# Optimization experiments

Measured on AMD Instinct MI355X. Metric: run time of the kernel, lower is better.

## Reference

```python
import jax, jax.numpy as jnp
import numpy as np

D = 512
H = 16
DH = D // H
N = 1024
R0 = 10.0
K_ITER = 20
LAM = 1.0


def _ln(x, w=None, b=None, eps=1e-5):
    m = x.mean(-1, keepdims=True)
    v = ((x - m) ** 2).mean(-1, keepdims=True)
    y = (x - m) * jax.lax.rsqrt(v + eps)
    if w is not None:
        y = y * w + b
    return y


def setup_inputs() -> dict:
    key = jax.random.key(0)
    ks = jax.random.split(key, 24)
    s = 1.0 / np.sqrt(D)
    inp = {
        'h': jax.random.normal(ks[0], (N, D), jnp.float32),
        'x_res': jax.random.normal(ks[1], (N, 3), jnp.float32) * 5.0,
        'mu': jax.random.uniform(ks[2], (H, N), jnp.float32, 0.1, 1.0),
        'nu': jax.random.uniform(ks[3], (H, N), jnp.float32, 0.1, 1.0),
        'log_u_prev': jnp.zeros((H, N), jnp.float32),
        'log_v_prev': jnp.zeros((H, N), jnp.float32),
        'w_rel_res': jax.random.normal(ks[4], (H, N, N), jnp.float32) * 0.1,
        'w_dist': jax.random.uniform(ks[5], (H,), jnp.float32),
        'pos_bins': jax.random.randint(ks[6], (N, N), 0, 68),
        'geo_gate': jax.random.uniform(ks[7], (H,), jnp.float32),
        'ln_attn_w': jnp.ones((D,), jnp.float32),
        'ln_attn_b': jnp.zeros((D,), jnp.float32),
        'Wq': jax.random.normal(ks[8], (D, D), jnp.float32) * s,
        'Wk': jax.random.normal(ks[9], (D, D), jnp.float32) * s,
        'Wv': jax.random.normal(ks[10], (D, D), jnp.float32) * s,
        'Wg': jax.random.normal(ks[11], (D, D), jnp.float32) * s,
        'Wo': jax.random.normal(ks[12], (D, D), jnp.float32) * s,
        'gamma': jax.random.normal(ks[13], (H,), jnp.float32) * 0.01,
        'ln_ff_w': jnp.ones((D,), jnp.float32),
        'ln_ff_b': jnp.zeros((D,), jnp.float32),
        'W1': jax.random.normal(ks[14], (D, 4 * D), jnp.float32) * s,
        'W3': jax.random.normal(ks[15], (D, 4 * D), jnp.float32) * s,
        'W2': jax.random.normal(ks[16], (4 * D, D), jnp.float32) / np.sqrt(4 * D),
    }
    return inp


def reference(h, x_res, mu, nu, log_u_prev, log_v_prev, w_rel_res, w_dist,
              pos_bins, geo_gate, ln_attn_w, ln_attn_b, Wq, Wk, Wv, Wg, Wo,
              gamma, ln_ff_w, ln_ff_b, W1, W3, W2):
    n = h.shape[0]
    h_n = _ln(h, ln_attn_w, ln_attn_b)
    # projections -> (H, N, d_h)
    Q = (h_n @ Wq).reshape(n, H, DH).transpose(1, 0, 2)
    K = (h_n @ Wk).reshape(n, H, DH).transpose(1, 0, 2)
    V = (h_n @ Wv).reshape(n, H, DH).transpose(1, 0, 2)
    G = (h_n @ Wg).reshape(n, H, DH).transpose(1, 0, 2)
    Q_ln = _ln(Q)
    K_ln = _ln(K)
    content = -jnp.einsum('hid,hjd->hij', Q_ln, K_ln) / np.sqrt(DH)
    pos_bias = w_rel_res  # precomputed (H, N, N)
    d2 = ((x_res[:, None, :] - x_res[None, :, :]) ** 2).sum(-1)
    dist = jnp.sqrt(jnp.maximum(d2, 1e-12))
    f_dist = dist / (R0 + dist)
    eff_w = geo_gate * w_dist
    C = content + pos_bias + eff_w[:, None, None] * f_dist[None]
    # log-domain unbalanced Sinkhorn, per-head eps
    eps_h = jnp.array([0.5] * 4 + [1.0] * 4 + [2.0] * 4 + [4.0] * 4, jnp.float32)
    eps_b = eps_h[:, None, None]
    fac = (LAM / (LAM + eps_h))[:, None]  # (H, 1)
    log_mu = jnp.log(jnp.clip(mu, 1e-8))
    log_nu = jnp.log(jnp.clip(nu, 1e-8))
    M = -C / eps_b  # (H, N, N)

    def step(carry, _):
        lu, lv = carry
        lu = fac * (log_mu - jax.nn.logsumexp(M + lv[:, None, :], axis=2))
        lv = fac * (log_nu - jax.nn.logsumexp(M + lu[:, :, None], axis=1))
        return (lu, lv), None

    (log_u, log_v), _ = jax.lax.scan(jax.checkpoint(step),
                                     (log_u_prev, log_v_prev), None,
                                     length=K_ITER)
    # transport plan and outputs
    T = jnp.exp(M + log_u[:, :, None] + log_v[:, None, :])
    T_norm = T / (T.sum(-1, keepdims=True) + 1e-8)
    o = jax.nn.sigmoid(G) * jnp.einsum('hij,hjd->hid', T_norm, V)
    o = o.transpose(1, 0, 2).reshape(n, D)
    h = h + o @ Wo
    x_centroid = jnp.einsum('hij,jc->hic', T_norm, x_res)  # (H, N, 3)
    delta = x_res[None] - x_centroid
    x_res = x_res + jnp.einsum('h,hnc->nc', gamma, delta)
    # SwiGLU FFN
    ff = _ln(h, ln_ff_w, ln_ff_b)
    h = h + (jax.nn.silu(ff @ W1) * (ff @ W3)) @ W2
    return h, x_res, log_u, log_v
```

## Files before the change

### kernel.cpp

```cpp
#include <hip/hip_runtime.h>
#include <math.h>

#define NTOK 1024
#define DDIM 512

using short8 = __attribute__((ext_vector_type(8))) short;
using f32x4  = __attribute__((ext_vector_type(4))) float;

__device__ __forceinline__ float4 ld4(const float* p){ return *(const float4*)p; }
__device__ __forceinline__ void st4(float* p, float4 v){ *(float4*)p = v; }
__device__ __forceinline__ unsigned short bf16r(float x) {
  unsigned int u = __float_as_uint(x);
  u += 0x7fffu + ((u >> 16) & 1u);
  return (unsigned short)(u >> 16);
}
__device__ __forceinline__ float bf16f(unsigned short h) {
  return __uint_as_float(((unsigned int)h) << 16);
}
__device__ __forceinline__ f32x4 mfma16(short8 a, short8 b, f32x4 c) {
  return __builtin_amdgcn_mfma_f32_16x16x32_bf16(a, b, c, 0, 0, 0);
}

__global__ __launch_bounds__(256) void ln_rows(const float* __restrict__ x,
    const float* __restrict__ w, const float* __restrict__ b, float* __restrict__ y) {
  int row = blockIdx.x, t = threadIdx.x;
  const float* xr = x + ((size_t)row << 9);
  float v0 = xr[t], v1 = xr[t + 256];
  float s = v0 + v1, q = v0*v0 + v1*v1;
  #pragma unroll
  for (int off = 1; off < 64; off <<= 1) { s += __shfl_xor(s, off); q += __shfl_xor(q, off); }
  __shared__ float ls[4], lq[4], mb[2];
  int wv = t >> 6;
  if ((t & 63) == 0) { ls[wv] = s; lq[wv] = q; }
  __syncthreads();
  if (t == 0) {
    float S = ls[0]+ls[1]+ls[2]+ls[3];
    float Q = lq[0]+lq[1]+lq[2]+lq[3];
    float m = S * (1.f/512.f);
    float var = Q * (1.f/512.f) - m*m;
    mb[0] = m; mb[1] = 1.f / sqrtf(var + 1e-5f);
  }
  __syncthreads();
  float m = mb[0], inv = mb[1];
  float* yr = y + ((size_t)row << 9);
  yr[t]       = (v0 - m) * inv * w[t] + b[t];
  yr[t + 256] = (v1 - m) * inv * w[t + 256] + b[t + 256];
}

struct C4 {
  const float *S0, *S1, *S2, *S3;
  unsigned short *D0, *D1, *D2, *D3;
};
__global__ __launch_bounds__(256) void convT(C4 p, int K, int N) {
  __shared__ unsigned short Th[64][68];
  __shared__ unsigned short Tl[64][68];
  int z = blockIdx.z;
  const float* src = (z==0)?p.S0:(z==1)?p.S1:(z==2)?p.S2:p.S3;
  unsigned short* dst = (z==0)?p.D0:(z==1)?p.D1:(z==2)?p.D2:p.D3;
  int nt = blockIdx.x << 6, kt = blockIdx.y << 6;
  int t = threadIdx.x;
  int r = t >> 4, c4 = (t & 15) << 2;
  #pragma unroll
  for (int pp = 0; pp < 4; ++pp) {
    int kk = r + (pp << 4);
    float4 v = ld4(src + (size_t)(kt + kk) * N + nt + c4);
    float vv[4] = {v.x, v.y, v.z, v.w};
    #pragma unroll
    for (int i = 0; i < 4; ++i) {
      unsigned short h = bf16r(vv[i]);
      Th[c4 + i][kk] = h;
      Tl[c4 + i][kk] = bf16r(vv[i] - bf16f(h));
    }
  }
  __syncthreads();
  size_t loff = (size_t)N * K;
  #pragma unroll
  for (int pp = 0; pp < 4; ++pp) {
    int nn = r + (pp << 4);
    ushort4 oh, ol;
    oh.x = Th[nn][c4]; oh.y = Th[nn][c4+1]; oh.z = Th[nn][c4+2]; oh.w = Th[nn][c4+3];
    ol.x = Tl[nn][c4]; ol.y = Tl[nn][c4+1]; ol.z = Tl[nn][c4+2]; ol.w = Tl[nn][c4+3];
    *(ushort4*)(dst + (size_t)(nt + nn) * K + kt + c4) = oh;
    *(ushort4*)(dst + loff + (size_t)(nt + nn) * K + kt + c4) = ol;
  }
}

struct P4 {
  const unsigned short *W0, *W1, *W2, *W3;
  float *C0, *C1, *C2, *C3;
};
template<int MODE>
__global__ __launch_bounds__(256) void gemm_mfma(const float* __restrict__ A,
    P4 p, int Kd, int Nd, int kwin) {
  __shared__ unsigned short Ash[64][72];
  __shared__ unsigned short Asl[64][72];
  __shared__ unsigned short Bsh[64][72];
  __shared__ unsigned short Bsl[64][72];
  int t = threadIdx.x;
  int z = blockIdx.z;
  const unsigned short* W = (z==0)?p.W0:(z==1)?p.W1:(z==2)?p.W2:p.W3;
  float* C = (z==0)?p.C0:(z==1)?p.C1:(z==2)?p.C2:p.C3;
  const unsigned short* Wl = W + (size_t)Nd * Kd;
  int bm = blockIdx.y << 6, bn = blockIdx.x << 6;
  int wid = t >> 6, lane = t & 63;
  int wm = wid >> 1, wn = wid & 1;
  int lr = lane & 15, lk = lane >> 4;
  int r0 = t >> 3, ks = (t & 7) << 3;
  int kbeg = kwin ? z * kwin : 0;
  int kend = kwin ? kbeg + kwin : Kd;
  f32x4 acc[2][2];
  #pragma unroll
  for (int i = 0; i < 2; ++i)
    #pragma unroll
    for (int j = 0; j < 2; ++j)
      #pragma unroll
      for (int r = 0; r < 4; ++r) acc[i][j][r] = 0.f;
  for (int k0 = kbeg; k0 < kend; k0 += 64) {
    float4 a00 = ld4(A + (size_t)(bm + r0) * Kd + k0 + ks);
    float4 a01 = ld4(A + (size_t)(bm + r0) * Kd + k0 + ks + 4);
    float4 a10 = ld4(A + (size_t)(bm + r0 + 32) * Kd + k0 + ks);
    float4 a11 = ld4(A + (size_t)(bm + r0 + 32) * Kd + k0 + ks + 4);
    uint4 b0h = *(const uint4*)(W  + (size_t)(bn + r0) * Kd + k0 + ks);
    uint4 b1h = *(const uint4*)(W  + (size_t)(bn + r0 + 32) * Kd + k0 + ks);
    uint4 b0l = *(const uint4*)(Wl + (size_t)(bn + r0) * Kd + k0 + ks);
    uint4 b1l = *(const uint4*)(Wl + (size_t)(bn + r0 + 32) * Kd + k0 + ks);
    __syncthreads();
    {
      float va[8] = {a00.x,a00.y,a00.z,a00.w,a01.x,a01.y,a01.z,a01.w};
      short8 h8, l8;
      #pragma unroll
      for (int i = 0; i < 8; ++i) {
        unsigned short h = bf16r(va[i]);
        h8[i] = (short)h; l8[i] = (short)bf16r(va[i] - bf16f(h));
      }
      *(short8*)&Ash[r0][ks] = h8;
      *(short8*)&Asl[r0][ks] = l8;
    }
    {
      float va[8] = {a10.x,a10.y,a10.z,a10.w,a11.x,a11.y,a11.z,a11.w};
      short8 h8, l8;
      #pragma unroll
      for (int i = 0; i < 8; ++i) {
        unsigned short h = bf16r(va[i]);
        h8[i] = (short)h; l8[i] = (short)bf16r(va[i] - bf16f(h));
      }
      *(short8*)&Ash[r0 + 32][ks] = h8;
      *(short8*)&Asl[r0 + 32][ks] = l8;
    }
    *(uint4*)&Bsh[r0][ks] = b0h;
    *(uint4*)&Bsh[r0 + 32][ks] = b1h;
    *(uint4*)&Bsl[r0][ks] = b0l;
    *(uint4*)&Bsl[r0 + 32][ks] = b1l;
    __syncthreads();
    #pragma unroll
    for (int s = 0; s < 2; ++s) {
      short8 ah0 = *(const short8*)&Ash[wm*32 + lr][s*32 + lk*8];
      short8 ah1 = *(const short8*)&Ash[wm*32 + 16 + lr][s*32 + lk*8];
      short8 al0 = *(const short8*)&Asl[wm*32 + lr][s*32 + lk*8];
      short8 al1 = *(const short8*)&Asl[wm*32 + 16 + lr][s*32 + lk*8];
      short8 bh0 = *(const short8*)&Bsh[wn*32 + lr][s*32 + lk*8];
      short8 bh1 = *(const short8*)&Bsh[wn*32 + 16 + lr][s*32 + lk*8];
      short8 bl0 = *(const short8*)&Bsl[wn*32 + lr][s*32 + lk*8];
      short8 bl1 = *(const short8*)&Bsl[wn*32 + 16 + lr][s*32 + lk*8];
      acc[0][0] = mfma16(ah0, bh0, acc[0][0]);
      acc[0][1] = mfma16(ah0, bh1, acc[0][1]);
      acc[1][0] = mfma16(ah1, bh0, acc[1][0]);
      acc[1][1] = mfma16(ah1, bh1, acc[1][1]);
      acc[0][0] = mfma16(al0, bh0, acc[0][0]);
      acc[0][1] = mfma16(al0, bh1, acc[0][1]);
      acc[1][0] = mfma16(al1, bh0, acc[1][0]);
      acc[1][1] = mfma16(al1, bh1, acc[1][1]);
      acc[0][0] = mfma16(ah0, bl0, acc[0][0]);
      acc[0][1] = mfma16(ah0, bl1, acc[0][1]);
      acc[1][0] = mfma16(ah1, bl0, acc[1][0]);
      acc[1][1] = mfma16(ah1, bl1, acc[1][1]);
    }
  }
  #pragma unroll
  for (int fm = 0; fm < 2; ++fm)
    #pragma unroll
    for (int fn = 0; fn < 2; ++fn) {
      int n = bn + wn*32 + fn*16 + lr;
      #pragma unroll
      for (int r = 0; r < 4; ++r) {
        int m = bm + wm*32 + fm*16 + lk*4 + r;
        float v = acc[fm][fn][r];
        if (MODE == 0) {
          if (z < 3) C[(((size_t)(n >> 5) << 10) + m) * 32 + (n & 31)] = v;
          else       C[(size_t)m * Nd + n] = v;
        } else {
          C[(size_t)m * Nd + n] = v;
        }
      }
    }
}

__global__ __launch_bounds__(256) void qk_ln(float* __restrict__ Q, float* __restrict__ K) {
  float* P = blockIdx.y ? K : Q;
  int t = threadIdx.x;
  int row = blockIdx.x * 8 + (t >> 5);
  int l = t & 31;
  float* p = P + ((size_t)row << 5);
  float x = p[l];
  float s = x, q = x*x;
  #pragma unroll
  for (int off = 16; off; off >>= 1) { s += __shfl_xor(s, off, 32); q += __shfl_xor(q, off, 32); }
  float m = s * (1.f/32.f);
  float var = q * (1.f/32.f) - m*m;
  float inv = 1.f / sqrtf(var + 1e-5f);
  p[l] = (x - m) * inv;
}

__global__ __launch_bounds__(256) void build_M(const float* __restrict__ Qln,
    const float* __restrict__ Kln, const float* __restrict__ wrel,
    const float* __restrict__ xres, const float* __restrict__ wdist,
    const float* __restrict__ ggate, short* __restrict__ Mq) {
  int jt = blockIdx.x, it = blockIdx.y, h = blockIdx.z;
  int t = threadIdx.x;
  __shared__ float Qs[64][44], Ks[64][44];
  __shared__ float xi[64][4], xj[64][4];
  #pragma unroll
  for (int rep = 0; rep < 2; ++rep) {
    int idx = t + (rep << 8);
    int rr = idx >> 3, dq = (idx & 7) << 2;
    st4(&Qs[rr][dq], ld4(Qln + ((((size_t)h << 10) + (it << 6) + rr) << 5) + dq));
    st4(&Ks[rr][dq], ld4(Kln + ((((size_t)h << 10) + (jt << 6) + rr) << 5) + dq));
  }
  if (t < 64) {
    int gi = (it << 6) + t, gj = (jt << 6) + t;
    xi[t][0] = xres[gi*3]; xi[t][1] = xres[gi*3+1]; xi[t][2] = xres[gi*3+2];
    xj[t][0] = xres[gj*3]; xj[t][1] = xres[gj*3+1]; xj[t][2] = xres[gj*3+2];
  }
  __syncthreads();
  int g = h >> 2;
  float inv_eps = 2.0f / (float)(1 << g);
  float effw = ggate[h] * wdist[h];
  int tr = t >> 4, tc = t & 15;
  float acc[4][4] = {};
  #pragma unroll
  for (int d0 = 0; d0 < 32; d0 += 4) {
    float4 q4[4], k4[4];
    #pragma unroll
    for (int a = 0; a < 4; ++a) q4[a] = ld4(&Qs[(tr << 2) + a][d0]);
    #pragma unroll
    for (int bq = 0; bq < 4; ++bq) k4[bq] = ld4(&Ks[(tc << 2) + bq][d0]);
    #pragma unroll
    for (int a = 0; a < 4; ++a)
      #pragma unroll
      for (int bq = 0; bq < 4; ++bq)
        acc[a][bq] += q4[a].x*k4[bq].x + q4[a].y*k4[bq].y + q4[a].z*k4[bq].z + q4[a].w*k4[bq].w;
  }
  const float is32 = 0.17677669529663687f;
  #pragma unroll
  for (int a = 0; a < 4; ++a) {
    int il = (tr << 2) + a;
    int i = (it << 6) + il;
    float xa0 = xi[il][0], xa1 = xi[il][1], xa2 = xi[il][2];
    size_t base = ((size_t)h << 20) + ((size_t)i << 10) + (jt << 6) + (tc << 2);
    float4 w4 = ld4(wrel + base);
    short o16[4];
    #pragma unroll
    for (int bq = 0; bq < 4; ++bq) {
      int jl = (tc << 2) + bq;
      float dx = xa0 - xj[jl][0], dy = xa1 - xj[jl][1], dz = xa2 - xj[jl][2];
      float d2 = dx*dx + dy*dy + dz*dz;
      float dist = sqrtf(fmaxf(d2, 1e-12f));
      float f = dist / (10.0f + dist);
      float wv = (bq==0)?w4.x:(bq==1)?w4.y:(bq==2)?w4.z:w4.w;
      float m = (acc[a][bq] * is32 - wv - effw * f) * inv_eps;
      o16[bq] = (short)__float2int_rn(fminf(fmaxf(m * 256.f, -32000.f), 32000.f));
    }
    short4 q4o; q4o.x = o16[0]; q4o.y = o16[1]; q4o.z = o16[2]; q4o.w = o16[3];
    *(short4*)(Mq + base) = q4o;
  }
}

__global__ __launch_bounds__(256) void sink_iter16(const short* __restrict__ Mq,
    const float* __restrict__ lvb, const float* __restrict__ mu,
    float* __restrict__ lu_out, float* __restrict__ part) {
  __shared__ float lds[4][1024];
  __shared__ float logmu[32];
  int bt = blockIdx.x, h = blockIdx.y;
  int t = threadIdx.x, w = t >> 6, lane = t & 63;
  int g = h >> 2;
  float eps = 0.5f * (float)(1 << g);
  float fac = 1.f / (1.f + eps);
  const float qs = 1.f / 256.f;
  int rowbase = bt << 5;
  if (t < 32) logmu[t] = __logf(fmaxf(mu[(h << 10) + rowbase + t], 1e-8f));
  const short* Mh = Mq + ((size_t)h << 20);
  int ib = rowbase + (w << 3);
  short8 qa[8], qb[8];
  #pragma unroll
  for (int k = 0; k < 8; ++k) {
    const short* row = Mh + ((size_t)(ib + k) << 10) + (lane << 3);
    qa[k] = *(const short8*)row;
    qb[k] = *(const short8*)(row + 512);
  }
  float4 lv4[2][2], env[2][2];
  #pragma unroll
  for (int c = 0; c < 2; ++c) {
    const float* lp = lvb + (h << 10) + (c << 9) + (lane << 3);
    lv4[c][0] = ld4(lp);
    lv4[c][1] = ld4(lp + 4);
    #pragma unroll
    for (int hv = 0; hv < 2; ++hv) {
      env[c][hv].x = __expf(-lv4[c][hv].x); env[c][hv].y = __expf(-lv4[c][hv].y);
      env[c][hv].z = __expf(-lv4[c][hv].z); env[c][hv].w = __expf(-lv4[c][hv].w);
    }
  }
  float4 colacc[2][2];
  #pragma unroll
  for (int c = 0; c < 2; ++c)
    #pragma unroll
    for (int hv = 0; hv < 2; ++hv) colacc[c][hv] = make_float4(0.f,0.f,0.f,0.f);
  #pragma unroll
  for (int k = 0; k < 8; ++k) {
    short8 q0 = qa[k], q1 = qb[k];
    float4 e[2][2];
    e[0][0].x = __expf((float)q0[0]*qs + lv4[0][0].x);
    e[0][0].y = __expf((float)q0[1]*qs + lv4[0][0].y);
    e[0][0].z = __expf((float)q0[2]*qs + lv4[0][0].z);
    e[0][0].w = __expf((float)q0[3]*qs + lv4[0][0].w);
    e[0][1].x = __expf((float)q0[4]*qs + lv4[0][1].x);
    e[0][1].y = __expf((float)q0[5]*qs + lv4[0][1].y);
    e[0][1].z = __expf((float)q0[6]*qs + lv4[0][1].z);
    e[0][1].w = __expf((float)q0[7]*qs + lv4[0][1].w);
    e[1][0].x = __expf((float)q1[0]*qs + lv4[1][0].x);
    e[1][0].y = __expf((float)q1[1]*qs + lv4[1][0].y);
    e[1][0].z = __expf((float)q1[2]*qs + lv4[1][0].z);
    e[1][0].w = __expf((float)q1[3]*qs + lv4[1][0].w);
    e[1][1].x = __expf((float)q1[4]*qs + lv4[1][1].x);
    e[1][1].y = __expf((float)q1[5]*qs + lv4[1][1].y);
    e[1][1].z = __expf((float)q1[6]*qs + lv4[1][1].z);
    e[1][1].w = __expf((float)q1[7]*qs + lv4[1][1].w);
    float racc = ((e[0][0].x + e[0][0].y) + (e[0][0].z + e[0][0].w))
               + ((e[0][1].x + e[0][1].y) + (e[0][1].z + e[0][1].w))
               + ((e[1][0].x + e[1][0].y) + (e[1][0].z + e[1][0].w))
               + ((e[1][1].x + e[1][1].y) + (e[1][1].z + e[1][1].w));
    #pragma unroll
    for (int off = 1; off < 64; off <<= 1) racc += __shfl_xor(racc, off);
    float lu = fac * (logmu[(w << 3) + k] - __logf(racc));
    if (lane == 0) lu_out[(h << 10) + ib + k] = lu;
    float s1 = __expf(lu);
    #pragma unroll
    for (int c = 0; c < 2; ++c)
      #pragma unroll
      for (int hv = 0; hv < 2; ++hv) {
        colacc[c][hv].x += s1 * (e[c][hv].x * env[c][hv].x);
        colacc[c][hv].y += s1 * (e[c][hv].y * env[c][hv].y);
        colacc[c][hv].z += s1 * (e[c][hv].z * env[c][hv].z);
        colacc[c][hv].w += s1 * (e[c][hv].w * env[c][hv].w);
      }
  }
  #pragma unroll
  for (int c = 0; c < 2; ++c) {
    st4(&lds[w][(c << 9) + (lane << 3)], colacc[c][0]);
    st4(&lds[w][(c << 9) + (lane << 3) + 4], colacc[c][1]);
  }
  __syncthreads();
  #pragma unroll
  for (int c = 0; c < 4; ++c) {
    int j = t + (c << 8);
    float v = (lds[0][j] + lds[1][j]) + (lds[2][j] + lds[3][j]);
    part[(((size_t)(h << 5) + bt) << 10) + j] = v;
  }
}

__global__ __launch_bounds__(256) void sink_fin(const float* __restrict__ part,
    const float* __restrict__ nu, float* __restrict__ lvb) {
  int cx = blockIdx.x, h = blockIdx.y;
  int t = threadIdx.x;
  int g = h >> 2;
  float eps = 0.5f * (float)(1 << g);
  float fac = 1.f / (1.f + eps);
  int j = (cx << 8) + t;
  float sum = 0.f;
  #pragma unroll 8
  for (int b = 0; b < 32; ++b)
    sum += part[(((size_t)(h << 5) + b) << 10) + j];
  float lv = fac * (__logf(fmaxf(nu[(h << 10) + j], 1e-8f)) - __logf(sum));
  lvb[(h << 10) + j] = lv;
}

__global__ __launch_bounds__(256) void attn_out_v3(const short* __restrict__ Mq,
    const float* __restrict__ lu_g, const float* __restrict__ lv_g,
    const float* __restrict__ V, const float* __restrict__ G,
    const float* __restrict__ xres, float* __restrict__ o_buf, float* __restrict__ xc) {
  __shared__ short mslab[32][1024];
  __shared__ float lv_s[1024];
  __shared__ float Vs[64][40];
  int rb = blockIdx.x, h = blockIdx.y;
  int t = threadIdx.x;
  int rowbase = rb << 5;
  const short* Mh = Mq + ((size_t)h << 20) + ((size_t)rowbase << 10);
  #pragma unroll
  for (int rep = 0; rep < 16; ++rep) {
    int idx = (rep << 8) + t;
    int rr = idx >> 7, c8 = (idx & 127) << 3;
    *(short8*)&mslab[rr][c8] = *(const short8*)(Mh + ((size_t)rr << 10) + c8);
  }
  ((float4*)lv_s)[t] = ld4(lv_g + (h << 10) + (t << 2));
  int r = t >> 3, cg = t & 7;
  float lu_r = lu_g[(h << 10) + rowbase + r];
  const float qs = 1.f / 256.f;
  float accO[4] = {0.f, 0.f, 0.f, 0.f};
  float rs = 0.f, accX = 0.f;
  for (int jt = 0; jt < 16; ++jt) {
    __syncthreads();
    {
      int vr = t >> 2, dq = (t & 3) << 3;
      const float* vp = V + ((((size_t)h << 10) + (jt << 6) + vr) << 5) + dq;
      st4(&Vs[vr][dq], ld4(vp));
      st4(&Vs[vr][dq + 4], ld4(vp + 4));
    }
    if (t < 64) {
      int j = (jt << 6) + t;
      Vs[t][32] = xres[j*3]; Vs[t][33] = xres[j*3+1]; Vs[t][34] = xres[j*3+2];
    }
    __syncthreads();
    const short* mrow = &mslab[r][jt << 6];
    const float* lvp = &lv_s[jt << 6];
    #pragma unroll 8
    for (int jj = 0; jj < 64; ++jj) {
      float e = __expf((float)mrow[jj] * qs + lu_r + lvp[jj]);
      float4 v4 = ld4(&Vs[jj][cg << 2]);
      accO[0] += e*v4.x; accO[1] += e*v4.y; accO[2] += e*v4.z; accO[3] += e*v4.w;
      rs += e;
      accX += e * Vs[jj][32 + cg];
    }
  }
  float inv = 1.f / (rs + 1e-8f);
  int i = rowbase + r;
  size_t ga = ((size_t)i << 9) + (h << 5) + (cg << 2);
  float4 g4 = ld4(G + ga);
  float4 o;
  o.x = accO[0]*inv / (1.f + __expf(-g4.x));
  o.y = accO[1]*inv / (1.f + __expf(-g4.y));
  o.z = accO[2]*inv / (1.f + __expf(-g4.z));
  o.w = accO[3]*inv / (1.f + __expf(-g4.w));
  st4(o_buf + ga, o);
  if (cg < 3)
    xc[((size_t)((h << 10) + i)) * 3 + cg] = accX * inv;
}

__global__ void x_update(const float* __restrict__ xres, const float* __restrict__ xc,
    const float* __restrict__ gamma, float* __restrict__ xout) {
  int idx = blockIdx.x * 256 + threadIdx.x;
  if (idx >= 3072) return;
  float x = xres[idx];
  float s = x;
  #pragma unroll
  for (int hh = 0; hh < 16; ++hh) s += gamma[hh] * (x - xc[(size_t)hh * 3072 + idx]);
  xout[idx] = s;
}

__global__ __launch_bounds__(256) void silu_mul(const float* __restrict__ P1,
    const float* __restrict__ P3, float* __restrict__ AB) {
  int i = (blockIdx.x * 256 + threadIdx.x) << 2;
  float4 a = ld4(P1 + i), b = ld4(P3 + i);
  float4 o;
  o.x = a.x / (1.f + __expf(-a.x)) * b.x;
  o.y = a.y / (1.f + __expf(-a.y)) * b.y;
  o.z = a.z / (1.f + __expf(-a.z)) * b.z;
  o.w = a.w / (1.f + __expf(-a.w)) * b.w;
  st4(AB + i, o);
}

__global__ __launch_bounds__(256) void add3(const float* __restrict__ a,
    const float* __restrict__ b, const float* __restrict__ c, float* __restrict__ o) {
  int i = (blockIdx.x * 256 + threadIdx.x) << 2;
  float4 va = ld4(a + i), vb = ld4(b + i), vc = ld4(c + i);
  st4(o + i, make_float4(va.x+vb.x+vc.x, va.y+vb.y+vc.y, va.z+vb.z+vc.z, va.w+vb.w+vc.w));
}

extern "C" void kernel_launch(void* const* d_in, const int* in_sizes, int n_in,
                              void* d_out, int out_size, void* d_ws, size_t ws_size,
                              hipStream_t stream) {
  const float* h_in    = (const float*)d_in[0];
  const float* x_res   = (const float*)d_in[1];
  const float* mu      = (const float*)d_in[2];
  const float* nu      = (const float*)d_in[3];
  const float* lv_prev = (const float*)d_in[5];
  const float* wrel    = (const float*)d_in[6];
  const float* wdist   = (const float*)d_in[7];
  const float* ggate   = (const float*)d_in[9];
  const float* lnaw    = (const float*)d_in[10];
  const float* lnab    = (const float*)d_in[11];
  const float* Wq      = (const float*)d_in[12];
  const float* Wk      = (const float*)d_in[13];
  const float* Wv      = (const float*)d_in[14];
  const float* Wg      = (const float*)d_in[15];
  const float* Wo      = (const float*)d_in[16];
  const float* gamma   = (const float*)d_in[17];
  const float* lnfw    = (const float*)d_in[18];
  const float* lnfb    = (const float*)d_in[19];
  const float* W1      = (const float*)d_in[20];
  const float* W3      = (const float*)d_in[21];
  const float* W2      = (const float*)d_in[22];

  float* out = (float*)d_out;
  float* OUT_H  = out;
  float* OUT_X  = out + 524288;
  float* OUT_LU = out + 527360;
  float* OUT_LV = out + 543744;

  if (ws_size < (size_t)19988480 * sizeof(float)) return;
  float* ws   = (float*)d_ws;
  float* Qb   = ws;
  float* Kb   = ws + 524288;
  float* Vb   = ws + 1048576;
  float* Gb   = ws + 1572864;
  float* Mb   = ws + 2097152;
  float* part = ws + 18874368;
  float* xcb  = ws + 19922944;
  short* Mq   = (short*)Mb;
  float* h_n = Mb;
  unsigned short* WqT = (unsigned short*)(Mb + 524288);
  unsigned short* WkT = (unsigned short*)(Mb + 786432);
  unsigned short* WvT = (unsigned short*)(Mb + 1048576);
  unsigned short* WgT = (unsigned short*)(Mb + 1310720);
  float* P1 = Mb;
  float* P3 = Mb + 2097152;
  float* ABb = Mb + 4194304;
  unsigned short* W1T = (unsigned short*)(Mb + 6291456);
  unsigned short* W3T = (unsigned short*)(Mb + 7340032);
  unsigned short* W2T = (unsigned short*)(Mb + 8388608);
  unsigned short* WoT = (unsigned short*)(Mb + 9437184);
  float* Pa = Mb + 9699328;
  float* Pb = Mb + 10223616;
  float* o_buf = part;
  float* h2  = Qb;
  float* ffb = Kb;

  ln_rows<<<NTOK, 256, 0, stream>>>(h_in, lnaw, lnab, h_n);
  {
    C4 c = { Wq, Wk, Wv, Wg, WqT, WkT, WvT, WgT };
    convT<<<dim3(8, 8, 4), 256, 0, stream>>>(c, 512, 512);
  }
  {
    P4 p = { WqT, WkT, WvT, WgT, Qb, Kb, Vb, Gb };
    gemm_mfma<0><<<dim3(8, 16, 4), 256, 0, stream>>>(h_n, p, 512, 512, 0);
  }
  qk_ln<<<dim3(2048, 2), 256, 0, stream>>>(Qb, Kb);
  build_M<<<dim3(16, 16, 16), 256, 0, stream>>>(Qb, Kb, wrel, x_res, wdist, ggate, Mq);
  hipMemcpyAsync(OUT_LV, lv_prev, 16384 * sizeof(float), hipMemcpyDeviceToDevice, stream);
  for (int it = 0; it < 20; ++it) {
    sink_iter16<<<dim3(32, 16), 256, 0, stream>>>(Mq, OUT_LV, mu, OUT_LU, part);
    sink_fin<<<dim3(4, 16), 256, 0, stream>>>(part, nu, OUT_LV);
  }
  attn_out_v3<<<dim3(32, 16), 256, 0, stream>>>(Mq, OUT_LU, OUT_LV, Vb, Gb, x_res, o_buf, xcb);
  x_update<<<12, 256, 0, stream>>>(x_res, xcb, gamma, OUT_X);

  {
    C4 c = { Wo, nullptr, nullptr, nullptr, WoT, nullptr, nullptr, nullptr };
    convT<<<dim3(8, 8, 1), 256, 0, stream>>>(c, 512, 512);
  }
  {
    C4 c = { W1, W3, nullptr, nullptr, W1T, W3T, nullptr, nullptr };
    convT<<<dim3(32, 8, 2), 256, 0, stream>>>(c, 512, 2048);
  }
  {
    C4 c = { W2, nullptr, nullptr, nullptr, W2T, nullptr, nullptr, nullptr };
    convT<<<dim3(8, 32, 1), 256, 0, stream>>>(c, 2048, 512);
  }
  {
    P4 p = { WoT, WoT, nullptr, nullptr, Pa, Pb, nullptr, nullptr };
    gemm_mfma<1><<<dim3(8, 16, 2), 256, 0, stream>>>(o_buf, p, 512, 512, 256);
  }
  add3<<<512, 256, 0, stream>>>(Pa, Pb, h_in, h2);
  ln_rows<<<NTOK, 256, 0, stream>>>(h2, lnfw, lnfb, ffb);
  {
    P4 p = { W1T, W3T, nullptr, nullptr, P1, P3, nullptr, nullptr };
    gemm_mfma<1><<<dim3(32, 16, 2), 256, 0, stream>>>(ffb, p, 512, 2048, 0);
  }
  silu_mul<<<2048, 256, 0, stream>>>(P1, P3, ABb);
  {
    P4 p = { W2T, W2T, nullptr, nullptr, Pa, Pb, nullptr, nullptr };
    gemm_mfma<1><<<dim3(8, 16, 2), 256, 0, stream>>>(ABb, p, 2048, 512, 1024);
  }
  add3<<<512, 256, 0, stream>>>(Pa, Pb, h2, OUT_H);
}
```

Baseline: 492.3 us.

## Halve Sinkhorn rows per block and precompute bf16 exp slab in attention output

Measured after the change: 478.1 us. 2.9% less time.

```diff
diff --git a/kernel.cpp b/kernel.cpp
--- a/kernel.cpp
+++ b/kernel.cpp
@@ -275,24 +275,23 @@
   }
 }
 
-__global__ __launch_bounds__(256) void sink_iter16(const short* __restrict__ Mq,
+__global__ __launch_bounds__(256) void sink_iter8(const short* __restrict__ Mq,
     const float* __restrict__ lvb, const float* __restrict__ mu,
     float* __restrict__ lu_out, float* __restrict__ part) {
   __shared__ float lds[4][1024];
-  __shared__ float logmu[32];
+  __shared__ float logmu[16];
   int bt = blockIdx.x, h = blockIdx.y;
   int t = threadIdx.x, w = t >> 6, lane = t & 63;
-  int g = h >> 2;
-  float eps = 0.5f * (float)(1 << g);
+  float eps = 0.5f * (float)(1 << (h >> 2));
   float fac = 1.f / (1.f + eps);
   const float qs = 1.f / 256.f;
-  int rowbase = bt << 5;
-  if (t < 32) logmu[t] = __logf(fmaxf(mu[(h << 10) + rowbase + t], 1e-8f));
+  int rowbase = bt << 4;
+  if (t < 16) logmu[t] = __logf(fmaxf(mu[(h << 10) + rowbase + t], 1e-8f));
   const short* Mh = Mq + ((size_t)h << 20);
-  int ib = rowbase + (w << 3);
-  short8 qa[8], qb[8];
-  #pragma unroll
-  for (int k = 0; k < 8; ++k) {
+  int ib = rowbase + (w << 2);
+  short8 qa[4], qb[4];
+  #pragma unroll
+  for (int k = 0; k < 4; ++k) {
     const short* row = Mh + ((size_t)(ib + k) << 10) + (lane << 3);
     qa[k] = *(const short8*)row;
     qb[k] = *(const short8*)(row + 512);
@@ -315,7 +314,7 @@
     #pragma unroll
     for (int hv = 0; hv < 2; ++hv) colacc[c][hv] = make_float4(0.f,0.f,0.f,0.f);
   #pragma unroll
-  for (int k = 0; k < 8; ++k) {
+  for (int k = 0; k < 4; ++k) {
     short8 q0 = qa[k], q1 = qb[k];
     float4 e[2][2];
     e[0][0].x = __expf((float)q0[0]*qs + lv4[0][0].x);
@@ -340,7 +339,7 @@
                + ((e[1][1].x + e[1][1].y) + (e[1][1].z + e[1][1].w));
     #pragma unroll
     for (int off = 1; off < 64; off <<= 1) racc += __shfl_xor(racc, off);
-    float lu = fac * (logmu[(w << 3) + k] - __logf(racc));
+    float lu = fac * (logmu[(w << 2) + k] - __logf(racc));
     if (lane == 0) lu_out[(h << 10) + ib + k] = lu;
     float s1 = __expf(lu);
     #pragma unroll
@@ -363,7 +362,7 @@
   for (int c = 0; c < 4; ++c) {
     int j = t + (c << 8);
     float v = (lds[0][j] + lds[1][j]) + (lds[2][j] + lds[3][j]);
-    part[(((size_t)(h << 5) + bt) << 10) + j] = v;
+    part[(((size_t)(h << 6) + bt) << 10) + j] = v;
   }
 }
 
@@ -371,39 +370,46 @@
     const float* __restrict__ nu, float* __restrict__ lvb) {
   int cx = blockIdx.x, h = blockIdx.y;
   int t = threadIdx.x;
-  int g = h >> 2;
-  float eps = 0.5f * (float)(1 << g);
+  float eps = 0.5f * (float)(1 << (h >> 2));
   float fac = 1.f / (1.f + eps);
   int j = (cx << 8) + t;
   float sum = 0.f;
-  #pragma unroll 8
-  for (int b = 0; b < 32; ++b)
-    sum += part[(((size_t)(h << 5) + b) << 10) + j];
+  #pragma unroll 16
+  for (int b = 0; b < 64; ++b)
+    sum += part[(((size_t)(h << 6) + b) << 10) + j];
   float lv = fac * (__logf(fmaxf(nu[(h << 10) + j], 1e-8f)) - __logf(sum));
   lvb[(h << 10) + j] = lv;
 }
 
-__global__ __launch_bounds__(256) void attn_out_v3(const short* __restrict__ Mq,
+__global__ __launch_bounds__(256) void attn_out_v4(const short* __restrict__ Mq,
     const float* __restrict__ lu_g, const float* __restrict__ lv_g,
     const float* __restrict__ V, const float* __restrict__ G,
     const float* __restrict__ xres, float* __restrict__ o_buf, float* __restrict__ xc) {
-  __shared__ short mslab[32][1024];
+  __shared__ unsigned short eslab[32][1032];
   __shared__ float lv_s[1024];
+  __shared__ float lu_s[32];
   __shared__ float Vs[64][40];
   int rb = blockIdx.x, h = blockIdx.y;
   int t = threadIdx.x;
   int rowbase = rb << 5;
+  ((float4*)lv_s)[t] = ld4(lv_g + (h << 10) + (t << 2));
+  if (t < 32) lu_s[t] = lu_g[(h << 10) + rowbase + t];
+  __syncthreads();
   const short* Mh = Mq + ((size_t)h << 20) + ((size_t)rowbase << 10);
+  const float qs = 1.f / 256.f;
   #pragma unroll
   for (int rep = 0; rep < 16; ++rep) {
     int idx = (rep << 8) + t;
     int rr = idx >> 7, c8 = (idx & 127) << 3;
-    *(short8*)&mslab[rr][c8] = *(const short8*)(Mh + ((size_t)rr << 10) + c8);
-  }
-  ((float4*)lv_s)[t] = ld4(lv_g + (h << 10) + (t << 2));
+    short8 m8 = *(const short8*)(Mh + ((size_t)rr << 10) + c8);
+    float lur = lu_s[rr];
+    short8 e8;
+    #pragma unroll
+    for (int i = 0; i < 8; ++i)
+      e8[i] = (short)bf16r(__expf((float)m8[i] * qs + lur + lv_s[c8 + i]));
+    *(short8*)&eslab[rr][c8] = e8;
+  }
   int r = t >> 3, cg = t & 7;
-  float lu_r = lu_g[(h << 10) + rowbase + r];
-  const float qs = 1.f / 256.f;
   float accO[4] = {0.f, 0.f, 0.f, 0.f};
   float rs = 0.f, accX = 0.f;
   for (int jt = 0; jt < 16; ++jt) {
@@ -419,11 +425,10 @@
       Vs[t][32] = xres[j*3]; Vs[t][33] = xres[j*3+1]; Vs[t][34] = xres[j*3+2];
     }
     __syncthreads();
-    const short* mrow = &mslab[r][jt << 6];
-    const float* lvp = &lv_s[jt << 6];
+    const unsigned short* erow = &eslab[r][jt << 6];
     #pragma unroll 8
     for (int jj = 0; jj < 64; ++jj) {
-      float e = __expf((float)mrow[jj] * qs + lu_r + lvp[jj]);
+      float e = bf16f(erow[jj]);
       float4 v4 = ld4(&Vs[jj][cg << 2]);
       accO[0] += e*v4.x; accO[1] += e*v4.y; accO[2] += e*v4.z; accO[3] += e*v4.w;
       rs += e;
@@ -546,10 +551,10 @@
   build_M<<<dim3(16, 16, 16), 256, 0, stream>>>(Qb, Kb, wrel, x_res, wdist, ggate, Mq);
   hipMemcpyAsync(OUT_LV, lv_prev, 16384 * sizeof(float), hipMemcpyDeviceToDevice, stream);
   for (int it = 0; it < 20; ++it) {
-    sink_iter16<<<dim3(32, 16), 256, 0, stream>>>(Mq, OUT_LV, mu, OUT_LU, part);
+    sink_iter8<<<dim3(64, 16), 256, 0, stream>>>(Mq, OUT_LV, mu, OUT_LU, part);
     sink_fin<<<dim3(4, 16), 256, 0, stream>>>(part, nu, OUT_LV);
   }
-  attn_out_v3<<<dim3(32, 16), 256, 0, stream>>>(Mq, OUT_LU, OUT_LV, Vb, Gb, x_res, o_buf, xcb);
+  attn_out_v4<<<dim3(32, 16), 256, 0, stream>>>(Mq, OUT_LU, OUT_LV, Vb, Gb, x_res, o_buf, xcb);
   x_update<<<12, 256, 0, stream>>>(x_res, xcb, gamma, OUT_X);
 
   {
```
